# Kernel optimization log

Hardware: AMD Instinct MI355X
Metric: run time of the kernel (lower is better)

## Reference

```python
import jax, jax.numpy as jnp
import numpy as np

IN_UNITS = 128
N_DRUG, N_DIS, N_EDGE = 10000, 5000, 2000000


def setup_inputs() -> dict:
    key = jax.random.key(0)
    ks = jax.random.split(key, 10)
    s1 = 1.0 / np.sqrt(2 * IN_UNITS)
    s2 = 1.0 / np.sqrt(128)
    s3 = 1.0 / np.sqrt(64)
    return {
        "drug_feat": jax.random.normal(ks[0], (N_DRUG, IN_UNITS), dtype=jnp.float32),
        "dis_feat": jax.random.normal(ks[1], (N_DIS, IN_UNITS), dtype=jnp.float32),
        "edge_index": jax.random.randint(ks[2], (2, N_EDGE), 0, N_DIS, dtype=jnp.int64),
        "W1": jax.random.uniform(ks[3], (128, 2 * IN_UNITS), jnp.float32, -s1, s1),
        "b1": jax.random.uniform(ks[4], (128,), jnp.float32, -s1, s1),
        "W2": jax.random.uniform(ks[5], (64, 128), jnp.float32, -s2, s2),
        "b2": jax.random.uniform(ks[6], (64,), jnp.float32, -s2, s2),
        "W3": jax.random.uniform(ks[7], (1, 64), jnp.float32, -s3, s3),
        "b3": jax.random.uniform(ks[8], (1,), jnp.float32, -s3, s3),
    }


def reference(drug_feat, dis_feat, edge_index, W1, b1, W2, b2, W3, b3):
    # Gather endpoint features and concat along feature dim: [E, 2*in_units]
    edge_feat = jnp.concatenate(
        (drug_feat[edge_index[0]], dis_feat[edge_index[1]]), axis=1
    )
    # 3-layer MLP (Dropout is identity in eval mode)
    h = jax.nn.relu(edge_feat @ W1.T + b1)  # [E, 128]
    h = jax.nn.relu(h @ W2.T + b2)          # [E, 64]
    return h @ W3.T + b3                     # [E, 1]
```

## Files before the change

kernel.cpp:

```cpp
#include <hip/hip_runtime.h>


typedef __bf16 bf16x8 __attribute__((ext_vector_type(8)));
typedef unsigned short u16x8 __attribute__((ext_vector_type(8)));
typedef float f32x4 __attribute__((ext_vector_type(4)));

static __device__ __forceinline__ unsigned short f2b(float f) {
  unsigned int u = __builtin_bit_cast(unsigned int, f);
  u += 0x7FFFu + ((u >> 16) & 1u);
  return (unsigned short)(u >> 16);
}

static __device__ __forceinline__ f32x4 mfma_bf16(u16x8 a, u16x8 b, f32x4 c) {
  return __builtin_amdgcn_mfma_f32_16x16x32_bf16(
      __builtin_bit_cast(bf16x8, a), __builtin_bit_cast(bf16x8, b), c, 0, 0, 0);
}

__global__ void cvt_tables(const float* __restrict__ a, const float* __restrict__ b,
                           unsigned short* __restrict__ oa, unsigned short* __restrict__ ob,
                           int na, int nb) {
  const int t = blockIdx.x * blockDim.x + threadIdx.x;
  const int ta = na >> 3;
  const float* src;
  unsigned short* dst;
  int i;
  if (t < ta) {
    src = a; dst = oa; i = t;
  } else {
    i = t - ta;
    if (i >= (nb >> 3)) return;
    src = b; dst = ob;
  }
  const float4 f0 = *(const float4*)(src + i * 8);
  const float4 f1 = *(const float4*)(src + i * 8 + 4);
  u16x8 v;
  v[0] = f2b(f0.x); v[1] = f2b(f0.y); v[2] = f2b(f0.z); v[3] = f2b(f0.w);
  v[4] = f2b(f1.x); v[5] = f2b(f1.y); v[6] = f2b(f1.z); v[7] = f2b(f1.w);
  *(u16x8*)(dst + i * 8) = v;
}

__global__ void cvt_weights(const float* __restrict__ W1, const float* __restrict__ W2,
                            unsigned short* __restrict__ o1, unsigned short* __restrict__ o2) {
  const int t = blockIdx.x * blockDim.x + threadIdx.x;
  if (t < 4096) {
    const int l = t & 63, kt = (t >> 6) & 7, ut = t >> 9;
    const int n = 16 * ut + (l & 15), k0 = 32 * kt + 8 * (l >> 4);
    const float* src = W1 + n * 256 + k0;
    u16x8 v;
#pragma unroll
    for (int j = 0; j < 8; ++j) v[j] = f2b(src[j]);
    *(u16x8*)(o1 + t * 8) = v;
  } else if (t < 5120) {
    const int u = t - 4096;
    const int l = u & 63, kt = (u >> 6) & 3, nt = u >> 8;
    const int n = 16 * nt + (l & 15), k0 = 32 * kt + 8 * (l >> 4);
    const float* src = W2 + n * 128 + k0;
    u16x8 v;
#pragma unroll
    for (int j = 0; j < 8; ++j) v[j] = f2b(src[j]);
    *(u16x8*)(o2 + u * 8) = v;
  }
}

__global__ __launch_bounds__(256, 4) void mlp_fused(
    const unsigned short* __restrict__ drugB, const unsigned short* __restrict__ disB,
    const int* __restrict__ eidx, const unsigned short* __restrict__ w1frag,
    const unsigned short* __restrict__ w2frag, const float* __restrict__ b1,
    const float* __restrict__ b2, const float* __restrict__ W3,
    const float* __restrict__ b3, float* __restrict__ out, int E) {
  __shared__ __align__(16) unsigned char smem[32768 + 1024];
  unsigned char* Abase = smem;
  float* partials = (float*)(smem + 32768);

  const int tid = threadIdx.x;
  const int wn = tid >> 6;
  const int l = tid & 63;
  const int l15 = l & 15;
  const int lq = l >> 4;
  const int e0 = blockIdx.x * 64;

  {
    const int r = tid >> 2;
    const int q = tid & 3;
    int e = e0 + r;
    if (e >= E) e = E - 1;
    const int idx = (q < 2) ? eidx[e] : eidx[E + e];
    const unsigned short* src = ((q < 2) ? drugB : disB) + (long)idx * 128 + (q & 1) * 64;
    unsigned char* rowp = Abase + r * 512;
    const int base = q * 128;
    const int swz = (r & 7) << 4;
#pragma unroll
    for (int c = 0; c < 8; ++c) {
      const u16x8 v = *(const u16x8*)(src + c * 8);
      *(u16x8*)(rowp + ((base + c * 16) ^ swz)) = v;
    }
  }

  u16x8 w2f[4];
#pragma unroll
  for (int kt = 0; kt < 4; ++kt)
    w2f[kt] = *(const u16x8*)(w2frag + ((wn * 4 + kt) * 64 + l) * 8);
  const float4 b1v0 = *(const float4*)(b1 + 32 * wn + 4 * lq);
  const float4 b1v1 = *(const float4*)(b1 + 32 * wn + 16 + 4 * lq);
  const float4 b2v = *(const float4*)(b2 + 16 * wn + 4 * lq);
  const float4 w3v = *(const float4*)(W3 + 16 * wn + 4 * lq);
  __syncthreads();

  f32x4 acc1[2][4];
#pragma unroll
  for (int uti = 0; uti < 2; ++uti)
#pragma unroll
    for (int nt = 0; nt < 4; ++nt) acc1[uti][nt] = (f32x4){0.f, 0.f, 0.f, 0.f};

  const unsigned short* w1p = w1frag + ((2 * wn) * 512 + l) * 8;
  u16x8 nf0 = *(const u16x8*)(w1p);
  u16x8 nf1 = *(const u16x8*)(w1p + 512 * 8);
#pragma unroll
  for (int kt = 0; kt < 8; ++kt) {
    const u16x8 c0 = nf0, c1 = nf1;
    if (kt < 7) {
      nf0 = *(const u16x8*)(w1p + (kt + 1) * 64 * 8);
      nf1 = *(const u16x8*)(w1p + (512 + (kt + 1) * 64) * 8);
    }
#pragma unroll
    for (int nt = 0; nt < 4; ++nt) {
      const int e = 16 * nt + l15;
      const u16x8 b = *(const u16x8*)(Abase + e * 512 + ((64 * kt + 16 * lq) ^ ((e & 7) << 4)));
      acc1[0][nt] = mfma_bf16(c0, b, acc1[0][nt]);
      acc1[1][nt] = mfma_bf16(c1, b, acc1[1][nt]);
    }
  }
  __syncthreads();

#pragma unroll
  for (int uti = 0; uti < 2; ++uti) {
    const float4 bv = uti ? b1v1 : b1v0;
#pragma unroll
    for (int nt = 0; nt < 4; ++nt) {
      const int e = 16 * nt + l15;
      float h0 = acc1[uti][nt][0] + bv.x; h0 = h0 > 0.f ? h0 : 0.f;
      float h1 = acc1[uti][nt][1] + bv.y; h1 = h1 > 0.f ? h1 : 0.f;
      float h2 = acc1[uti][nt][2] + bv.z; h2 = h2 > 0.f ? h2 : 0.f;
      float h3 = acc1[uti][nt][3] + bv.w; h3 = h3 > 0.f ? h3 : 0.f;
      ushort4 hv;
      hv.x = f2b(h0); hv.y = f2b(h1); hv.z = f2b(h2); hv.w = f2b(h3);
      *(ushort4*)(Abase + e * 256 + ((64 * wn + 32 * uti + 8 * lq) ^ ((e & 7) << 4))) = hv;
    }
  }
  __syncthreads();

  f32x4 acc2[4];
#pragma unroll
  for (int nt = 0; nt < 4; ++nt) acc2[nt] = (f32x4){0.f, 0.f, 0.f, 0.f};
#pragma unroll
  for (int kt = 0; kt < 4; ++kt) {
#pragma unroll
    for (int nt = 0; nt < 4; ++nt) {
      const int e = 16 * nt + l15;
      const u16x8 b = *(const u16x8*)(Abase + e * 256 + ((64 * kt + 16 * lq) ^ ((e & 7) << 4)));
      acc2[nt] = mfma_bf16(w2f[kt], b, acc2[nt]);
    }
  }

#pragma unroll
  for (int nt = 0; nt < 4; ++nt) {
    float h0 = acc2[nt][0] + b2v.x; h0 = h0 > 0.f ? h0 : 0.f;
    float h1 = acc2[nt][1] + b2v.y; h1 = h1 > 0.f ? h1 : 0.f;
    float h2 = acc2[nt][2] + b2v.z; h2 = h2 > 0.f ? h2 : 0.f;
    float h3 = acc2[nt][3] + b2v.w; h3 = h3 > 0.f ? h3 : 0.f;
    float s = h0 * w3v.x + h1 * w3v.y + h2 * w3v.z + h3 * w3v.w;
    s += __shfl_xor(s, 16, 64);
    s += __shfl_xor(s, 32, 64);
    if (l < 16) partials[wn * 64 + 16 * nt + l15] = s;
  }
  __syncthreads();

  if (tid < 64) {
    const int e = e0 + tid;
    if (e < E) {
      out[e] = partials[tid] + partials[64 + tid] + partials[128 + tid] +
               partials[192 + tid] + b3[0];
    }
  }
}

extern "C" void kernel_launch(void* const* d_in, const int* in_sizes, int n_in,
                              void* d_out, int out_size, void* d_ws, size_t ws_size,
                              hipStream_t stream) {
  const float* drug = (const float*)d_in[0];
  const float* dis = (const float*)d_in[1];
  const int* eidx = (const int*)d_in[2];
  const float* W1 = (const float*)d_in[3];
  const float* b1 = (const float*)d_in[4];
  const float* W2 = (const float*)d_in[5];
  const float* b2 = (const float*)d_in[6];
  const float* W3 = (const float*)d_in[7];
  const float* b3 = (const float*)d_in[8];
  float* out = (float*)d_out;

  const int na = in_sizes[0];
  const int nb = in_sizes[1];
  const int E = in_sizes[2] / 2;

  unsigned short* ws = (unsigned short*)d_ws;
  unsigned short* drugB = ws;
  unsigned short* disB = ws + na;
  unsigned short* w1f = ws + na + nb;
  unsigned short* w2f = w1f + 128 * 256;

  const int tct = (na + nb) >> 3;
  cvt_tables<<<(tct + 255) / 256, 256, 0, stream>>>(drug, dis, drugB, disB, na, nb);
  cvt_weights<<<20, 256, 0, stream>>>(W1, W2, w1f, w2f);

  const int grid = (E + 63) / 64;
  mlp_fused<<<grid, 256, 0, stream>>>(drugB, disB, eidx, w1f, w2f, b1, b2, W3, b3, out, E);
}
```

Baseline: 245.2 us.

## Retile fused MLP waves into 2x2 edge-by-unit grid and reorganize gather

```diff
diff --git a/kernel.cpp b/kernel.cpp
--- a/kernel.cpp
+++ b/kernel.cpp
@@ -68,119 +68,132 @@
     const unsigned short* __restrict__ w2frag, const float* __restrict__ b1,
     const float* __restrict__ b2, const float* __restrict__ W3,
     const float* __restrict__ b3, float* __restrict__ out, int E) {
-  __shared__ __align__(16) unsigned char smem[32768 + 1024];
+  __shared__ __align__(16) unsigned char smem[32768 + 512];
   unsigned char* Abase = smem;
   float* partials = (float*)(smem + 32768);
 
   const int tid = threadIdx.x;
-  const int wn = tid >> 6;
+  const int wv = tid >> 6;
+  const int wm = wv >> 1;
+  const int wn2 = wv & 1;
   const int l = tid & 63;
   const int l15 = l & 15;
   const int lq = l >> 4;
   const int e0 = blockIdx.x * 64;
 
   {
-    const int r = tid >> 2;
-    const int q = tid & 3;
-    int e = e0 + r;
+    const int q = wv;
+    int e = e0 + l;
     if (e >= E) e = E - 1;
-    const int idx = (q < 2) ? eidx[e] : eidx[E + e];
+    const int idx = eidx[(q >> 1) * E + e];
     const unsigned short* src = ((q < 2) ? drugB : disB) + (long)idx * 128 + (q & 1) * 64;
-    unsigned char* rowp = Abase + r * 512;
+    unsigned char* rowp = Abase + l * 512;
     const int base = q * 128;
-    const int swz = (r & 7) << 4;
+    const int swz = (l & 7) << 4;
 #pragma unroll
     for (int c = 0; c < 8; ++c) {
       const u16x8 v = *(const u16x8*)(src + c * 8);
       *(u16x8*)(rowp + ((base + c * 16) ^ swz)) = v;
     }
   }
-
-  u16x8 w2f[4];
-#pragma unroll
-  for (int kt = 0; kt < 4; ++kt)
-    w2f[kt] = *(const u16x8*)(w2frag + ((wn * 4 + kt) * 64 + l) * 8);
-  const float4 b1v0 = *(const float4*)(b1 + 32 * wn + 4 * lq);
-  const float4 b1v1 = *(const float4*)(b1 + 32 * wn + 16 + 4 * lq);
-  const float4 b2v = *(const float4*)(b2 + 16 * wn + 4 * lq);
-  const float4 w3v = *(const float4*)(W3 + 16 * wn + 4 * lq);
-  __syncthreads();
-
-  f32x4 acc1[2][4];
-#pragma unroll
-  for (int uti = 0; uti < 2; ++uti)
-#pragma unroll
-    for (int nt = 0; nt < 4; ++nt) acc1[uti][nt] = (f32x4){0.f, 0.f, 0.f, 0.f};
-
-  const unsigned short* w1p = w1frag + ((2 * wn) * 512 + l) * 8;
-  u16x8 nf0 = *(const u16x8*)(w1p);
-  u16x8 nf1 = *(const u16x8*)(w1p + 512 * 8);
+  __syncthreads();
+
+  f32x4 acc1[4][2];
+#pragma unroll
+  for (int uti = 0; uti < 4; ++uti) {
+    acc1[uti][0] = (f32x4){0.f, 0.f, 0.f, 0.f};
+    acc1[uti][1] = (f32x4){0.f, 0.f, 0.f, 0.f};
+  }
+  const unsigned short* w1p = w1frag + ((4 * wn2) * 512 + l) * 8;
+  u16x8 nf[4];
+#pragma unroll
+  for (int uti = 0; uti < 4; ++uti) nf[uti] = *(const u16x8*)(w1p + uti * 512 * 8);
 #pragma unroll
   for (int kt = 0; kt < 8; ++kt) {
-    const u16x8 c0 = nf0, c1 = nf1;
+    u16x8 cf[4];
+#pragma unroll
+    for (int uti = 0; uti < 4; ++uti) cf[uti] = nf[uti];
     if (kt < 7) {
-      nf0 = *(const u16x8*)(w1p + (kt + 1) * 64 * 8);
-      nf1 = *(const u16x8*)(w1p + (512 + (kt + 1) * 64) * 8);
-    }
-#pragma unroll
-    for (int nt = 0; nt < 4; ++nt) {
-      const int e = 16 * nt + l15;
+#pragma unroll
+      for (int uti = 0; uti < 4; ++uti)
+        nf[uti] = *(const u16x8*)(w1p + (uti * 512 + (kt + 1) * 64) * 8);
+    }
+#pragma unroll
+    for (int ntl = 0; ntl < 2; ++ntl) {
+      const int e = 32 * wm + 16 * ntl + l15;
       const u16x8 b = *(const u16x8*)(Abase + e * 512 + ((64 * kt + 16 * lq) ^ ((e & 7) << 4)));
-      acc1[0][nt] = mfma_bf16(c0, b, acc1[0][nt]);
-      acc1[1][nt] = mfma_bf16(c1, b, acc1[1][nt]);
-    }
-  }
-  __syncthreads();
-
-#pragma unroll
-  for (int uti = 0; uti < 2; ++uti) {
-    const float4 bv = uti ? b1v1 : b1v0;
-#pragma unroll
-    for (int nt = 0; nt < 4; ++nt) {
-      const int e = 16 * nt + l15;
-      float h0 = acc1[uti][nt][0] + bv.x; h0 = h0 > 0.f ? h0 : 0.f;
-      float h1 = acc1[uti][nt][1] + bv.y; h1 = h1 > 0.f ? h1 : 0.f;
-      float h2 = acc1[uti][nt][2] + bv.z; h2 = h2 > 0.f ? h2 : 0.f;
-      float h3 = acc1[uti][nt][3] + bv.w; h3 = h3 > 0.f ? h3 : 0.f;
+#pragma unroll
+      for (int uti = 0; uti < 4; ++uti) acc1[uti][ntl] = mfma_bf16(cf[uti], b, acc1[uti][ntl]);
+    }
+  }
+  __syncthreads();
+
+#pragma unroll
+  for (int uti = 0; uti < 4; ++uti) {
+    const float4 bv = *(const float4*)(b1 + 64 * wn2 + 16 * uti + 4 * lq);
+#pragma unroll
+    for (int ntl = 0; ntl < 2; ++ntl) {
+      const int e = 32 * wm + 16 * ntl + l15;
+      float h0 = acc1[uti][ntl][0] + bv.x; h0 = h0 > 0.f ? h0 : 0.f;
+      float h1 = acc1[uti][ntl][1] + bv.y; h1 = h1 > 0.f ? h1 : 0.f;
+      float h2 = acc1[uti][ntl][2] + bv.z; h2 = h2 > 0.f ? h2 : 0.f;
+      float h3 = acc1[uti][ntl][3] + bv.w; h3 = h3 > 0.f ? h3 : 0.f;
       ushort4 hv;
       hv.x = f2b(h0); hv.y = f2b(h1); hv.z = f2b(h2); hv.w = f2b(h3);
-      *(ushort4*)(Abase + e * 256 + ((64 * wn + 32 * uti + 8 * lq) ^ ((e & 7) << 4))) = hv;
-    }
-  }
-  __syncthreads();
-
-  f32x4 acc2[4];
-#pragma unroll
-  for (int nt = 0; nt < 4; ++nt) acc2[nt] = (f32x4){0.f, 0.f, 0.f, 0.f};
+      *(ushort4*)(Abase + e * 256 +
+                  ((32 * (4 * wn2 + uti) + 8 * lq) ^ ((e & 7) << 4))) = hv;
+    }
+  }
+
+  u16x8 w2fr[2][4];
+#pragma unroll
+  for (int j = 0; j < 2; ++j)
+#pragma unroll
+    for (int kt = 0; kt < 4; ++kt)
+      w2fr[j][kt] = *(const u16x8*)(w2frag + (((2 * wn2 + j) * 4 + kt) * 64 + l) * 8);
+  __syncthreads();
+
+  f32x4 acc2[2][2];
+#pragma unroll
+  for (int j = 0; j < 2; ++j) {
+    acc2[j][0] = (f32x4){0.f, 0.f, 0.f, 0.f};
+    acc2[j][1] = (f32x4){0.f, 0.f, 0.f, 0.f};
+  }
 #pragma unroll
   for (int kt = 0; kt < 4; ++kt) {
 #pragma unroll
-    for (int nt = 0; nt < 4; ++nt) {
-      const int e = 16 * nt + l15;
+    for (int ntl = 0; ntl < 2; ++ntl) {
+      const int e = 32 * wm + 16 * ntl + l15;
       const u16x8 b = *(const u16x8*)(Abase + e * 256 + ((64 * kt + 16 * lq) ^ ((e & 7) << 4)));
-      acc2[nt] = mfma_bf16(w2f[kt], b, acc2[nt]);
-    }
-  }
-
-#pragma unroll
-  for (int nt = 0; nt < 4; ++nt) {
-    float h0 = acc2[nt][0] + b2v.x; h0 = h0 > 0.f ? h0 : 0.f;
-    float h1 = acc2[nt][1] + b2v.y; h1 = h1 > 0.f ? h1 : 0.f;
-    float h2 = acc2[nt][2] + b2v.z; h2 = h2 > 0.f ? h2 : 0.f;
-    float h3 = acc2[nt][3] + b2v.w; h3 = h3 > 0.f ? h3 : 0.f;
-    float s = h0 * w3v.x + h1 * w3v.y + h2 * w3v.z + h3 * w3v.w;
+#pragma unroll
+      for (int j = 0; j < 2; ++j) acc2[j][ntl] = mfma_bf16(w2fr[j][kt], b, acc2[j][ntl]);
+    }
+  }
+
+  const float4 b2v0 = *(const float4*)(b2 + 32 * wn2 + 4 * lq);
+  const float4 b2v1 = *(const float4*)(b2 + 32 * wn2 + 16 + 4 * lq);
+  const float4 w3v0 = *(const float4*)(W3 + 32 * wn2 + 4 * lq);
+  const float4 w3v1 = *(const float4*)(W3 + 32 * wn2 + 16 + 4 * lq);
+#pragma unroll
+  for (int ntl = 0; ntl < 2; ++ntl) {
+    float h, s = 0.f;
+    h = acc2[0][ntl][0] + b2v0.x; s += (h > 0.f ? h : 0.f) * w3v0.x;
+    h = acc2[0][ntl][1] + b2v0.y; s += (h > 0.f ? h : 0.f) * w3v0.y;
+    h = acc2[0][ntl][2] + b2v0.z; s += (h > 0.f ? h : 0.f) * w3v0.z;
+    h = acc2[0][ntl][3] + b2v0.w; s += (h > 0.f ? h : 0.f) * w3v0.w;
+    h = acc2[1][ntl][0] + b2v1.x; s += (h > 0.f ? h : 0.f) * w3v1.x;
+    h = acc2[1][ntl][1] + b2v1.y; s += (h > 0.f ? h : 0.f) * w3v1.y;
+    h = acc2[1][ntl][2] + b2v1.z; s += (h > 0.f ? h : 0.f) * w3v1.z;
+    h = acc2[1][ntl][3] + b2v1.w; s += (h > 0.f ? h : 0.f) * w3v1.w;
     s += __shfl_xor(s, 16, 64);
     s += __shfl_xor(s, 32, 64);
-    if (l < 16) partials[wn * 64 + 16 * nt + l15] = s;
+    if (l < 16) partials[wn2 * 64 + 32 * wm + 16 * ntl + l15] = s;
   }
   __syncthreads();
 
   if (tid < 64) {
     const int e = e0 + tid;
-    if (e < E) {
-      out[e] = partials[tid] + partials[64 + tid] + partials[128 + tid] +
-               partials[192 + tid] + b3[0];
-    }
+    if (e < E) out[e] = partials[tid] + partials[64 + tid] + b3[0];
   }
 }
 
```

Measured after the change: 296.0 us. +20.7%, slower.

## Make MLP kernel persistent with register-prefetched gathers and resident W1 fragments

Applied to the files above, without the earlier changes.

```diff
diff --git a/kernel.cpp b/kernel.cpp
--- a/kernel.cpp
+++ b/kernel.cpp
@@ -62,125 +62,152 @@
   }
 }
 
-__global__ __launch_bounds__(256, 4) void mlp_fused(
+__global__ __launch_bounds__(256, 3) void mlp_fused(
     const unsigned short* __restrict__ drugB, const unsigned short* __restrict__ disB,
     const int* __restrict__ eidx, const unsigned short* __restrict__ w1frag,
     const unsigned short* __restrict__ w2frag, const float* __restrict__ b1,
     const float* __restrict__ b2, const float* __restrict__ W3,
     const float* __restrict__ b3, float* __restrict__ out, int E) {
-  __shared__ __align__(16) unsigned char smem[32768 + 1024];
+  __shared__ __align__(16) unsigned char smem[32768 + 16384 + 1024];
   unsigned char* Abase = smem;
-  float* partials = (float*)(smem + 32768);
+  unsigned char* Hbase = smem + 32768;
+  float* partials = (float*)(smem + 49152);
 
   const int tid = threadIdx.x;
   const int wn = tid >> 6;
   const int l = tid & 63;
   const int l15 = l & 15;
   const int lq = l >> 4;
-  const int e0 = blockIdx.x * 64;
-
+  const int T = (E + 63) >> 6;
+  const int stride = (int)gridDim.x;
+
+  u16x8 w1r[2][8];
   {
-    const int r = tid >> 2;
-    const int q = tid & 3;
-    int e = e0 + r;
-    if (e >= E) e = E - 1;
-    const int idx = (q < 2) ? eidx[e] : eidx[E + e];
-    const unsigned short* src = ((q < 2) ? drugB : disB) + (long)idx * 128 + (q & 1) * 64;
-    unsigned char* rowp = Abase + r * 512;
-    const int base = q * 128;
-    const int swz = (r & 7) << 4;
-#pragma unroll
-    for (int c = 0; c < 8; ++c) {
-      const u16x8 v = *(const u16x8*)(src + c * 8);
-      *(u16x8*)(rowp + ((base + c * 16) ^ swz)) = v;
-    }
-  }
-
-  u16x8 w2f[4];
-#pragma unroll
-  for (int kt = 0; kt < 4; ++kt)
-    w2f[kt] = *(const u16x8*)(w2frag + ((wn * 4 + kt) * 64 + l) * 8);
+    const unsigned short* w1p = w1frag + ((2 * wn) * 512 + l) * 8;
+#pragma unroll
+    for (int uti = 0; uti < 2; ++uti)
+#pragma unroll
+      for (int kt = 0; kt < 8; ++kt)
+        w1r[uti][kt] = *(const u16x8*)(w1p + (uti * 512 + kt * 64) * 8);
+  }
   const float4 b1v0 = *(const float4*)(b1 + 32 * wn + 4 * lq);
   const float4 b1v1 = *(const float4*)(b1 + 32 * wn + 16 + 4 * lq);
   const float4 b2v = *(const float4*)(b2 + 16 * wn + 4 * lq);
   const float4 w3v = *(const float4*)(W3 + 16 * wn + 4 * lq);
+  const float b3v = b3[0];
+
+  const int gq = wn;
+  const int gbase = gq * 128;
+  const int gswz = (l & 7) << 4;
+  unsigned char* growp = Abase + l * 512;
+
+  int t = blockIdx.x;
+  if (t >= T) return;
+
+  {
+    int e = t * 64 + l;
+    if (e >= E) e = E - 1;
+    const int idx = eidx[(gq >> 1) * E + e];
+    const unsigned short* src = ((gq < 2) ? drugB : disB) + (long)idx * 128 + (gq & 1) * 64;
+#pragma unroll
+    for (int c = 0; c < 8; ++c) {
+      const u16x8 v = *(const u16x8*)(src + c * 8);
+      *(u16x8*)(growp + ((gbase + c * 16) ^ gswz)) = v;
+    }
+  }
   __syncthreads();
 
-  f32x4 acc1[2][4];
-#pragma unroll
-  for (int uti = 0; uti < 2; ++uti)
-#pragma unroll
-    for (int nt = 0; nt < 4; ++nt) acc1[uti][nt] = (f32x4){0.f, 0.f, 0.f, 0.f};
-
-  const unsigned short* w1p = w1frag + ((2 * wn) * 512 + l) * 8;
-  u16x8 nf0 = *(const u16x8*)(w1p);
-  u16x8 nf1 = *(const u16x8*)(w1p + 512 * 8);
-#pragma unroll
-  for (int kt = 0; kt < 8; ++kt) {
-    const u16x8 c0 = nf0, c1 = nf1;
-    if (kt < 7) {
-      nf0 = *(const u16x8*)(w1p + (kt + 1) * 64 * 8);
-      nf1 = *(const u16x8*)(w1p + (512 + (kt + 1) * 64) * 8);
-    }
+  while (t < T) {
+    const int tn = t + stride;
+    u16x8 g[8];
+    {
+      const int tc = (tn < T) ? tn : t;
+      int e = tc * 64 + l;
+      if (e >= E) e = E - 1;
+      const int idx = eidx[(gq >> 1) * E + e];
+      const unsigned short* src = ((gq < 2) ? drugB : disB) + (long)idx * 128 + (gq & 1) * 64;
+#pragma unroll
+      for (int c = 0; c < 8; ++c) g[c] = *(const u16x8*)(src + c * 8);
+    }
+
+    f32x4 acc1[2][4];
+#pragma unroll
+    for (int uti = 0; uti < 2; ++uti)
+#pragma unroll
+      for (int nt = 0; nt < 4; ++nt) acc1[uti][nt] = (f32x4){0.f, 0.f, 0.f, 0.f};
+#pragma unroll
+    for (int kt = 0; kt < 8; ++kt) {
+#pragma unroll
+      for (int nt = 0; nt < 4; ++nt) {
+        const int e = 16 * nt + l15;
+        const u16x8 b =
+            *(const u16x8*)(Abase + e * 512 + ((64 * kt + 16 * lq) ^ ((e & 7) << 4)));
+        acc1[0][nt] = mfma_bf16(w1r[0][kt], b, acc1[0][nt]);
+        acc1[1][nt] = mfma_bf16(w1r[1][kt], b, acc1[1][nt]);
+      }
+    }
+    u16x8 w2f[4];
+#pragma unroll
+    for (int kt = 0; kt < 4; ++kt)
+      w2f[kt] = *(const u16x8*)(w2frag + ((wn * 4 + kt) * 64 + l) * 8);
+    __syncthreads();
+
+#pragma unroll
+    for (int c = 0; c < 8; ++c)
+      *(u16x8*)(growp + ((gbase + c * 16) ^ gswz)) = g[c];
+
+#pragma unroll
+    for (int uti = 0; uti < 2; ++uti) {
+      const float4 bv = uti ? b1v1 : b1v0;
+#pragma unroll
+      for (int nt = 0; nt < 4; ++nt) {
+        const int e = 16 * nt + l15;
+        float h0 = acc1[uti][nt][0] + bv.x; h0 = h0 > 0.f ? h0 : 0.f;
+        float h1 = acc1[uti][nt][1] + bv.y; h1 = h1 > 0.f ? h1 : 0.f;
+        float h2 = acc1[uti][nt][2] + bv.z; h2 = h2 > 0.f ? h2 : 0.f;
+        float h3 = acc1[uti][nt][3] + bv.w; h3 = h3 > 0.f ? h3 : 0.f;
+        ushort4 hv;
+        hv.x = f2b(h0); hv.y = f2b(h1); hv.z = f2b(h2); hv.w = f2b(h3);
+        *(ushort4*)(Hbase + e * 256 + ((64 * wn + 32 * uti + 8 * lq) ^ ((e & 7) << 4))) = hv;
+      }
+    }
+    __syncthreads();
+
+    f32x4 acc2[4];
+#pragma unroll
+    for (int nt = 0; nt < 4; ++nt) acc2[nt] = (f32x4){0.f, 0.f, 0.f, 0.f};
+#pragma unroll
+    for (int kt = 0; kt < 4; ++kt) {
+#pragma unroll
+      for (int nt = 0; nt < 4; ++nt) {
+        const int e = 16 * nt + l15;
+        const u16x8 b =
+            *(const u16x8*)(Hbase + e * 256 + ((64 * kt + 16 * lq) ^ ((e & 7) << 4)));
+        acc2[nt] = mfma_bf16(w2f[kt], b, acc2[nt]);
+      }
+    }
+
 #pragma unroll
     for (int nt = 0; nt < 4; ++nt) {
-      const int e = 16 * nt + l15;
-      const u16x8 b = *(const u16x8*)(Abase + e * 512 + ((64 * kt + 16 * lq) ^ ((e & 7) << 4)));
-      acc1[0][nt] = mfma_bf16(c0, b, acc1[0][nt]);
-      acc1[1][nt] = mfma_bf16(c1, b, acc1[1][nt]);
-    }
-  }
-  __syncthreads();
-
-#pragma unroll
-  for (int uti = 0; uti < 2; ++uti) {
-    const float4 bv = uti ? b1v1 : b1v0;
-#pragma unroll
-    for (int nt = 0; nt < 4; ++nt) {
-      const int e = 16 * nt + l15;
-      float h0 = acc1[uti][nt][0] + bv.x; h0 = h0 > 0.f ? h0 : 0.f;
-      float h1 = acc1[uti][nt][1] + bv.y; h1 = h1 > 0.f ? h1 : 0.f;
-      float h2 = acc1[uti][nt][2] + bv.z; h2 = h2 > 0.f ? h2 : 0.f;
-      float h3 = acc1[uti][nt][3] + bv.w; h3 = h3 > 0.f ? h3 : 0.f;
-      ushort4 hv;
-      hv.x = f2b(h0); hv.y = f2b(h1); hv.z = f2b(h2); hv.w = f2b(h3);
-      *(ushort4*)(Abase + e * 256 + ((64 * wn + 32 * uti + 8 * lq) ^ ((e & 7) << 4))) = hv;
-    }
-  }
-  __syncthreads();
-
-  f32x4 acc2[4];
-#pragma unroll
-  for (int nt = 0; nt < 4; ++nt) acc2[nt] = (f32x4){0.f, 0.f, 0.f, 0.f};
-#pragma unroll
-  for (int kt = 0; kt < 4; ++kt) {
-#pragma unroll
-    for (int nt = 0; nt < 4; ++nt) {
-      const int e = 16 * nt + l15;
-      const u16x8 b = *(const u16x8*)(Abase + e * 256 + ((64 * kt + 16 * lq) ^ ((e & 7) << 4)));
-      acc2[nt] = mfma_bf16(w2f[kt], b, acc2[nt]);
-    }
-  }
-
-#pragma unroll
-  for (int nt = 0; nt < 4; ++nt) {
-    float h0 = acc2[nt][0] + b2v.x; h0 = h0 > 0.f ? h0 : 0.f;
-    float h1 = acc2[nt][1] + b2v.y; h1 = h1 > 0.f ? h1 : 0.f;
-    float h2 = acc2[nt][2] + b2v.z; h2 = h2 > 0.f ? h2 : 0.f;
-    float h3 = acc2[nt][3] + b2v.w; h3 = h3 > 0.f ? h3 : 0.f;
-    float s = h0 * w3v.x + h1 * w3v.y + h2 * w3v.z + h3 * w3v.w;
-    s += __shfl_xor(s, 16, 64);
-    s += __shfl_xor(s, 32, 64);
-    if (l < 16) partials[wn * 64 + 16 * nt + l15] = s;
-  }
-  __syncthreads();
-
-  if (tid < 64) {
-    const int e = e0 + tid;
-    if (e < E) {
-      out[e] = partials[tid] + partials[64 + tid] + partials[128 + tid] +
-               partials[192 + tid] + b3[0];
-    }
+      float h0 = acc2[nt][0] + b2v.x; h0 = h0 > 0.f ? h0 : 0.f;
+      float h1 = acc2[nt][1] + b2v.y; h1 = h1 > 0.f ? h1 : 0.f;
+      float h2 = acc2[nt][2] + b2v.z; h2 = h2 > 0.f ? h2 : 0.f;
+      float h3 = acc2[nt][3] + b2v.w; h3 = h3 > 0.f ? h3 : 0.f;
+      float s = h0 * w3v.x + h1 * w3v.y + h2 * w3v.z + h3 * w3v.w;
+      s += __shfl_xor(s, 16, 64);
+      s += __shfl_xor(s, 32, 64);
+      if (l < 16) partials[wn * 64 + 16 * nt + l15] = s;
+    }
+    __syncthreads();
+
+    if (tid < 64) {
+      const int e = t * 64 + tid;
+      if (e < E) {
+        out[e] = partials[tid] + partials[64 + tid] + partials[128 + tid] +
+                 partials[192 + tid] + b3v;
+      }
+    }
+    t = tn;
   }
 }
 
@@ -212,6 +239,5 @@
   cvt_tables<<<(tct + 255) / 256, 256, 0, stream>>>(drug, dis, drugB, disB, na, nb);
   cvt_weights<<<20, 256, 0, stream>>>(W1, W2, w1f, w2f);
 
-  const int grid = (E + 63) / 64;
-  mlp_fused<<<grid, 256, 0, stream>>>(drugB, disB, eidx, w1f, w2f, b1, b2, W3, b3, out, E);
-}
+  mlp_fused<<<1536, 256, 0, stream>>>(drugB, disB, eidx, w1f, w2f, b1, b2, W3, b3, out, E);
+}
```

Result: slower. 417.2 us (+70.1%).
